# Kernel optimization log

Measured on AMD Instinct MI355X. Metric: run time of the kernel, lower is better.

The kernel has to match this reference:

```python
import jax, jax.numpy as jnp
import numpy as np

NUM_GRAPHS = 1024


def gcn_conv(x, src, dst, W, b, num_nodes):
    # PyG GCNConv: x' = D^{-1/2}(A+I)D^{-1/2} X W + b, self-loops added.
    h = x @ W  # [N, out]
    deg = jax.ops.segment_sum(jnp.ones_like(dst, dtype=h.dtype), dst, num_segments=num_nodes)
    dinv = jnp.where(deg > 0, jax.lax.rsqrt(deg), 0.0)
    norm = dinv[src] * dinv[dst]  # [E+N]
    msg = h[src] * norm[:, None]
    out = jax.ops.segment_sum(msg, dst, num_segments=num_nodes)
    return out + b


def setup_inputs() -> dict:
    key = jax.random.key(0)
    ks = jax.random.split(key, 16)
    N, E, F_IN, F_OUT = 100000, 1600000, 128, 256
    x = jax.random.normal(ks[0], (N, F_IN), dtype=jnp.float32)
    edge_index = jax.random.randint(ks[1], (2, E), 0, N, dtype=jnp.int64)
    batch = jnp.sort(jax.random.randint(ks[2], (N,), 0, NUM_GRAPHS, dtype=jnp.int64))

    def glorot(k, shape):
        lim = np.sqrt(6.0 / (shape[0] + shape[1]))
        return jax.random.uniform(k, shape, jnp.float32, -lim, lim)

    return {
        "x": x, "edge_index": edge_index, "batch": batch,
        "W1": glorot(ks[3], (F_IN, 16)), "b1": jnp.zeros((16,), jnp.float32),
        "W2": glorot(ks[4], (16, 32)), "b2": jnp.zeros((32,), jnp.float32),
        "W3": glorot(ks[5], (32, 64)), "b3": jnp.zeros((64,), jnp.float32),
        "L1_w": glorot(ks[6], (64, 256)), "L1_b": jnp.zeros((256,), jnp.float32),
        "L2_w": glorot(ks[7], (256, F_OUT)), "L2_b": jnp.zeros((F_OUT,), jnp.float32),
    }


def reference(x, edge_index, batch, W1, b1, W2, b2, W3, b3, L1_w, L1_b, L2_w, L2_b):
    N = x.shape[0]
    loops = jnp.arange(N, dtype=edge_index.dtype)
    src = jnp.concatenate([edge_index[0], loops])
    dst = jnp.concatenate([edge_index[1], loops])

    h = jax.nn.relu(gcn_conv(x, src, dst, W1, b1, N))
    h = jax.nn.relu(gcn_conv(h, src, dst, W2, b2, N))
    h = jax.nn.relu(gcn_conv(h, src, dst, W3, b3, N))

    pooled = jax.ops.segment_max(h, batch, num_segments=NUM_GRAPHS)  # [G, 64]
    pooled = jnp.where(jnp.isfinite(pooled), pooled, 0.0)  # empty segments -> 0

    z = jax.nn.relu(pooled @ L1_w + L1_b)
    return jax.nn.sigmoid(z @ L2_w + L2_b)
```

## Files before the change

### kernel.cpp

```cpp
#include <hip/hip_runtime.h>
#include <hip/hip_fp16.h>
#include <math.h>

#define NG 1024
#define EPB 2048
#define EPB_BIN 4096

static inline int cdiv_i(long long a, int b) { return (int)((a + b - 1) / b); }

union H8 { uint4 u; __half2 h[4]; };

__device__ inline void h8_to_f(uint4 uu, float* f) {
    H8 v; v.u = uu;
#pragma unroll
    for (int k = 0; k < 4; ++k) {
        float2 t = __half22float2(v.h[k]);
        f[2 * k] = t.x; f[2 * k + 1] = t.y;
    }
}
__device__ inline uint4 f_to_h8(const float* f) {
    H8 v;
#pragma unroll
    for (int k = 0; k < 4; ++k) v.h[k] = __floats2half2_rn(f[2 * k], f[2 * k + 1]);
    return v.u;
}

__global__ void zero_init(int* __restrict__ bcnt, unsigned* __restrict__ pooled) {
    int t = blockIdx.x * 256 + threadIdx.x;
    if (t < 256) bcnt[t] = 0;
    if (t < NG * 64) pooled[t] = 0;
}


__global__ void bucket_count(const int* __restrict__ dst, int* __restrict__ bcnt, int E) {
    __shared__ int h[256];
    int t = threadIdx.x;
    h[t] = 0;
    __syncthreads();
    int e0 = blockIdx.x * EPB;
#pragma unroll 4
    for (int k = 0; k < EPB / 256; ++k) {
        int e = e0 + k * 256 + t;
        if (e < E) atomicAdd(&h[dst[e] >> 9], 1);
    }
    __syncthreads();
    if (h[t] > 0) atomicAdd(&bcnt[t], h[t]);
}

__global__ void bucket_scan(const int* __restrict__ bcnt, int* __restrict__ bktbase,
                            int* __restrict__ bktcur, int* __restrict__ rowptr,
                            int NBKT, int N) {
    __shared__ int s[256];
    int t = threadIdx.x;
    int v = (t < NBKT) ? bcnt[t] : 0;
    s[t] = v;
    __syncthreads();
    for (int off = 1; off < 256; off <<= 1) {
        int u = (t >= off) ? s[t - off] : 0;
        __syncthreads();
        s[t] += u;
        __syncthreads();
    }
    int excl = s[t] - v;
    if (t < NBKT) { bktbase[t] = excl; bktcur[t] = excl; }
    if (t == 255) { bktbase[NBKT] = s[255]; rowptr[N] = s[255]; }
}

__global__ void bin_edges(const int* __restrict__ src, const int* __restrict__ dst,
                          int* __restrict__ bktcur, unsigned* __restrict__ binned, int E) {
    __shared__ int hist[256];
    __shared__ int sc[256];
    __shared__ int lofs[256];
    __shared__ int gbase[256];
    __shared__ int lcur[256];
    __shared__ unsigned stage[EPB_BIN];
    __shared__ int gaddr[EPB_BIN];
    int t = threadIdx.x;
    hist[t] = 0;
    __syncthreads();
    int e0 = blockIdx.x * EPB_BIN;
    int ne = E - e0; if (ne > EPB_BIN) ne = EPB_BIN;
    int myd[EPB_BIN / 256];
    int mys[EPB_BIN / 256];
#pragma unroll
    for (int k = 0; k < EPB_BIN / 256; ++k) {
        int e = e0 + k * 256 + t;
        if (e < E) {
            int d = dst[e];
            myd[k] = d;
            atomicAdd(&hist[d >> 9], 1);
        } else {
            myd[k] = -1;
        }
    }
#pragma unroll
    for (int k = 0; k < EPB_BIN / 256; ++k) {
        int e = e0 + k * 256 + t;
        mys[k] = (e < E) ? src[e] : 0;
    }
    __syncthreads();
    int v = hist[t];
    sc[t] = v;
    __syncthreads();
    for (int off = 1; off < 256; off <<= 1) {
        int u = (t >= off) ? sc[t - off] : 0;
        __syncthreads();
        sc[t] += u;
        __syncthreads();
    }
    lofs[t] = sc[t] - v;
    lcur[t] = sc[t] - v;
    if (v > 0) gbase[t] = atomicAdd(&bktcur[t], v);
    __syncthreads();
#pragma unroll
    for (int k = 0; k < EPB_BIN / 256; ++k) {
        int d = myd[k];
        if (d >= 0) {
            int b = d >> 9;
            int r = atomicAdd(&lcur[b], 1);
            stage[r] = ((unsigned)(d & 511) << 23) | (unsigned)mys[k];
            gaddr[r] = gbase[b] + (r - lofs[b]);
        }
    }
    __syncthreads();
    for (int j = t; j < ne; j += 256) binned[gaddr[j]] = stage[j];
}

__global__ void bucket_build(const int* __restrict__ bktbase, const unsigned* __restrict__ binned,
                             int* __restrict__ rowptr, float* __restrict__ dinv,
                             int* __restrict__ csr_src, int N) {
    __shared__ int degl[512];
    __shared__ int s[512];
    __shared__ int rp[512];
    __shared__ int cur[512];
    int t = threadIdx.x;
    int n0 = blockIdx.x << 9;
    degl[t] = 0;
    cur[t] = 0;
    __syncthreads();
    int base = bktbase[blockIdx.x], end = bktbase[blockIdx.x + 1];
    for (int j = base + t; j < end; j += 512) atomicAdd(&degl[binned[j] >> 23], 1);
    __syncthreads();
    int d = degl[t];
    s[t] = d;
    __syncthreads();
    for (int off = 1; off < 512; off <<= 1) {
        int u = (t >= off) ? s[t - off] : 0;
        __syncthreads();
        s[t] += u;
        __syncthreads();
    }
    rp[t] = base + s[t] - d;
    int i = n0 + t;
    if (i < N) {
        rowptr[i] = rp[t];
        dinv[i] = rsqrtf((float)(d + 1));
    }
    __syncthreads();
    for (int j = base + t; j < end; j += 512) {
        unsigned v = binned[j];
        int li = v >> 23;
        int slot = rp[li] + atomicAdd(&cur[li], 1);
        csr_src[slot] = (int)(v & 0x7FFFFFu);
    }
}

__global__ void gemm1(const float* __restrict__ x, const float* __restrict__ dinv,
                      const float* __restrict__ W, uint4* __restrict__ t1, int N) {
    __shared__ float Wl[128 * 16];
    int t = threadIdx.x;
    for (int k = t; k < 128 * 16; k += 256) Wl[k] = W[k];
    __syncthreads();
    int i = blockIdx.x * 256 + t;
    if (i >= N) return;
    const float4* x4 = (const float4*)(x + (size_t)i * 128);
    const float4* W4 = (const float4*)Wl;
    float4 a[4];
#pragma unroll
    for (int c = 0; c < 4; ++c) a[c] = make_float4(0.f, 0.f, 0.f, 0.f);
#pragma unroll 4
    for (int k4 = 0; k4 < 32; ++k4) {
        float4 v = x4[k4];
#pragma unroll
        for (int kk = 0; kk < 4; ++kk) {
            float xk = (kk == 0) ? v.x : (kk == 1) ? v.y : (kk == 2) ? v.z : v.w;
            const float4* Wr = W4 + (k4 * 4 + kk) * 4;
#pragma unroll
            for (int c = 0; c < 4; ++c) {
                float4 w = Wr[c];
                a[c].x += xk * w.x; a[c].y += xk * w.y;
                a[c].z += xk * w.z; a[c].w += xk * w.w;
            }
        }
    }
    float di = dinv[i];
    float f[16];
#pragma unroll
    for (int c = 0; c < 4; ++c) {
        f[4 * c + 0] = di * a[c].x; f[4 * c + 1] = di * a[c].y;
        f[4 * c + 2] = di * a[c].z; f[4 * c + 3] = di * a[c].w;
    }
    t1[(size_t)i * 2]     = f_to_h8(f);
    t1[(size_t)i * 2 + 1] = f_to_h8(f + 8);
}

__global__ void gather16_epi(const int* __restrict__ rowptr, const int* __restrict__ csr_src,
                             const uint4* __restrict__ hs, const float* __restrict__ dinv,
                             const float* __restrict__ b, uint4* __restrict__ out, int N) {
    int tid = blockIdx.x * 256 + threadIdx.x;
    int i = tid >> 1, c = tid & 1;
    if (i >= N) return;
    float acc[8];
    h8_to_f(hs[(size_t)i * 2 + c], acc);
    int j = rowptr[i], end = rowptr[i + 1];
    for (; j + 1 < end; j += 2) {
        int s0 = csr_src[j], s1 = csr_src[j + 1];
        uint4 u0 = hs[(size_t)s0 * 2 + c];
        uint4 u1 = hs[(size_t)s1 * 2 + c];
        float v0[8], v1[8];
        h8_to_f(u0, v0);
        h8_to_f(u1, v1);
#pragma unroll
        for (int k = 0; k < 8; ++k) acc[k] += v0[k] + v1[k];
    }
    if (j < end) {
        int s0 = csr_src[j];
        float v0[8];
        h8_to_f(hs[(size_t)s0 * 2 + c], v0);
#pragma unroll
        for (int k = 0; k < 8; ++k) acc[k] += v0[k];
    }
    float di = dinv[i];
#pragma unroll
    for (int k = 0; k < 8; ++k) acc[k] = di * fmaxf(di * acc[k] + b[c * 8 + k], 0.f);
    out[(size_t)i * 2 + c] = f_to_h8(acc);
}

__global__ void gather_gemm2(const int* __restrict__ rowptr, const int* __restrict__ csr_src,
                             const uint4* __restrict__ p1, const float* __restrict__ dinv,
                             const float* __restrict__ W, const float* __restrict__ b,
                             uint4* __restrict__ p2a, uint4* __restrict__ p2b, int N) {
    __shared__ float Wl[16 * 32];
    __shared__ float bl[32];
    int t = threadIdx.x;
    for (int k = t; k < 16 * 32; k += 256) Wl[k] = W[k];
    if (t < 32) bl[t] = b[t];
    __syncthreads();
    int i = blockIdx.x * 256 + t;
    if (i >= N) return;
    float f[16];
    h8_to_f(p1[(size_t)i * 2], f);
    h8_to_f(p1[(size_t)i * 2 + 1], f + 8);
    int j = rowptr[i], end = rowptr[i + 1];
    for (; j + 1 < end; j += 2) {
        int s0 = csr_src[j], s1 = csr_src[j + 1];
        uint4 a0 = p1[(size_t)s0 * 2], a1 = p1[(size_t)s0 * 2 + 1];
        uint4 b0 = p1[(size_t)s1 * 2], b1 = p1[(size_t)s1 * 2 + 1];
        float v[16], u[16];
        h8_to_f(a0, v); h8_to_f(a1, v + 8);
        h8_to_f(b0, u); h8_to_f(b1, u + 8);
#pragma unroll
        for (int k = 0; k < 16; ++k) f[k] += v[k] + u[k];
    }
    if (j < end) {
        int s0 = csr_src[j];
        float v[16];
        h8_to_f(p1[(size_t)s0 * 2], v);
        h8_to_f(p1[(size_t)s0 * 2 + 1], v + 8);
#pragma unroll
        for (int k = 0; k < 16; ++k) f[k] += v[k];
    }
    const float4* W4 = (const float4*)Wl;
    float4 a[8];
#pragma unroll
    for (int c = 0; c < 8; ++c) a[c] = make_float4(0.f, 0.f, 0.f, 0.f);
#pragma unroll
    for (int k = 0; k < 16; ++k) {
        float xk = f[k];
        const float4* Wr = W4 + k * 8;
#pragma unroll
        for (int c = 0; c < 8; ++c) {
            float4 w = Wr[c];
            a[c].x += xk * w.x; a[c].y += xk * w.y;
            a[c].z += xk * w.z; a[c].w += xk * w.w;
        }
    }
    float di = dinv[i];
    float o[32];
#pragma unroll
    for (int c = 0; c < 8; ++c) {
        o[4 * c + 0] = di * fmaxf(di * a[c].x + bl[4 * c + 0], 0.f);
        o[4 * c + 1] = di * fmaxf(di * a[c].y + bl[4 * c + 1], 0.f);
        o[4 * c + 2] = di * fmaxf(di * a[c].z + bl[4 * c + 2], 0.f);
        o[4 * c + 3] = di * fmaxf(di * a[c].w + bl[4 * c + 3], 0.f);
    }
    p2a[(size_t)i * 2]     = f_to_h8(o);
    p2a[(size_t)i * 2 + 1] = f_to_h8(o + 8);
    p2b[(size_t)i * 2]     = f_to_h8(o + 16);
    p2b[(size_t)i * 2 + 1] = f_to_h8(o + 24);
}

__global__ void gather_gemm3_pool(const int* __restrict__ rowptr, const int* __restrict__ csr_src,
                                  const uint4* __restrict__ p2a, const uint4* __restrict__ p2b,
                                  const float* __restrict__ dinv, const float* __restrict__ W,
                                  const float* __restrict__ b, const int* __restrict__ batch,
                                  unsigned* __restrict__ pooled, int N) {
    __shared__ float Wl[32 * 64];
    __shared__ float bl[64];
    __shared__ float fl[128][33];
    __shared__ float pl[128][65];
    __shared__ int bt[128];
    int t = threadIdx.x;
    for (int k = t; k < 32 * 64; k += 256) Wl[k] = W[k];
    if (t < 64) bl[t] = b[t];
    int i0 = blockIdx.x * 128;
    if (t < 128) {
        int i = i0 + t;
        bt[t] = (i < N) ? batch[i] : -1;
    }
    int il = t & 127, c = t >> 7;
    int i = i0 + il;
    if (i < N) {
        const uint4* P = c ? p2b : p2a;
        float acc[16];
        uint4 s0 = P[(size_t)i * 2], s1 = P[(size_t)i * 2 + 1];
        h8_to_f(s0, acc);
        h8_to_f(s1, acc + 8);
        int j = rowptr[i], end = rowptr[i + 1];
        for (; j + 1 < end; j += 2) {
            int n0 = csr_src[j], n1 = csr_src[j + 1];
            uint4 a0 = P[(size_t)n0 * 2], a1 = P[(size_t)n0 * 2 + 1];
            uint4 b0 = P[(size_t)n1 * 2], b1 = P[(size_t)n1 * 2 + 1];
            float v[16], u[16];
            h8_to_f(a0, v); h8_to_f(a1, v + 8);
            h8_to_f(b0, u); h8_to_f(b1, u + 8);
#pragma unroll
            for (int k = 0; k < 16; ++k) acc[k] += v[k] + u[k];
        }
        if (j < end) {
            int n0 = csr_src[j];
            float v[16];
            h8_to_f(P[(size_t)n0 * 2], v);
            h8_to_f(P[(size_t)n0 * 2 + 1], v + 8);
#pragma unroll
            for (int k = 0; k < 16; ++k) acc[k] += v[k];
        }
#pragma unroll
        for (int k = 0; k < 16; ++k) fl[il][c * 16 + k] = acc[k];
    }
    __syncthreads();
    if (i < N) {
        const float4* W4 = (const float4*)Wl;
        float4 a[8];
#pragma unroll
        for (int cc = 0; cc < 8; ++cc) a[cc] = make_float4(0.f, 0.f, 0.f, 0.f);
#pragma unroll 4
        for (int k = 0; k < 32; ++k) {
            float xk = fl[il][k];
            const float4* Wr = W4 + k * 16 + c * 8;
#pragma unroll
            for (int cc = 0; cc < 8; ++cc) {
                float4 w = Wr[cc];
                a[cc].x += xk * w.x; a[cc].y += xk * w.y;
                a[cc].z += xk * w.z; a[cc].w += xk * w.w;
            }
        }
        float di = dinv[i];
        int fb = c * 32;
#pragma unroll
        for (int cc = 0; cc < 8; ++cc) {
            pl[il][fb + 4 * cc + 0] = fmaxf(di * a[cc].x + bl[fb + 4 * cc + 0], 0.f);
            pl[il][fb + 4 * cc + 1] = fmaxf(di * a[cc].y + bl[fb + 4 * cc + 1], 0.f);
            pl[il][fb + 4 * cc + 2] = fmaxf(di * a[cc].z + bl[fb + 4 * cc + 2], 0.f);
            pl[il][fb + 4 * cc + 3] = fmaxf(di * a[cc].w + bl[fb + 4 * cc + 3], 0.f);
        }
    }
    __syncthreads();
    int f = t & 63, q = t >> 6;
    int prevb = -1;
    float run = 0.f;
    for (int k = 0; k < 32; ++k) {
        int il2 = q * 32 + k;
        int bg = bt[il2];
        if (bg < 0) break;
        float v = pl[il2][f];
        if (bg != prevb) {
            if (prevb >= 0) atomicMax(&pooled[prevb * 64 + f], __float_as_uint(run));
            prevb = bg;
            run = v;
        } else {
            run = fmaxf(run, v);
        }
    }
    if (prevb >= 0) atomicMax(&pooled[prevb * 64 + f], __float_as_uint(run));
}

__global__ void head4(const float* __restrict__ pooled, const float* __restrict__ w1,
                      const float* __restrict__ bb1, const float* __restrict__ w2,
                      const float* __restrict__ bb2, float* __restrict__ out) {
    __shared__ float p[4][64];
    __shared__ float z[4][256];
    int g0 = blockIdx.x * 4, t = threadIdx.x;
    p[t >> 6][t & 63] = pooled[(g0 + (t >> 6)) * 64 + (t & 63)];
    __syncthreads();
    float s[4];
#pragma unroll
    for (int q = 0; q < 4; ++q) s[q] = bb1[t];
    for (int k = 0; k < 64; ++k) {
        float w = w1[k * 256 + t];
#pragma unroll
        for (int q = 0; q < 4; ++q) s[q] += p[q][k] * w;
    }
#pragma unroll
    for (int q = 0; q < 4; ++q) z[q][t] = fmaxf(s[q], 0.f);
    __syncthreads();
    float s2[4];
#pragma unroll
    for (int q = 0; q < 4; ++q) s2[q] = bb2[t];
#pragma unroll 4
    for (int k = 0; k < 256; ++k) {
        float w = w2[k * 256 + t];
#pragma unroll
        for (int q = 0; q < 4; ++q) s2[q] += z[q][k] * w;
    }
#pragma unroll
    for (int q = 0; q < 4; ++q) out[(g0 + q) * 256 + t] = 1.f / (1.f + expf(-s2[q]));
}

extern "C" void kernel_launch(void* const* d_in, const int* in_sizes, int n_in,
                              void* d_out, int out_size, void* d_ws, size_t ws_size,
                              hipStream_t stream) {
    const float* x   = (const float*)d_in[0];
    const int* ei    = (const int*)d_in[1];
    const int* batch = (const int*)d_in[2];
    const float* W1  = (const float*)d_in[3];
    const float* b1  = (const float*)d_in[4];
    const float* W2  = (const float*)d_in[5];
    const float* b2  = (const float*)d_in[6];
    const float* W3  = (const float*)d_in[7];
    const float* b3  = (const float*)d_in[8];
    const float* L1w = (const float*)d_in[9];
    const float* L1b = (const float*)d_in[10];
    const float* L2w = (const float*)d_in[11];
    const float* L2b = (const float*)d_in[12];

    const int N = in_sizes[0] / 128;
    const int E = in_sizes[1] / 2;
    const int* srcp = ei;
    const int* dstp = ei + E;
    const int NB = cdiv_i(N, 256);
    const int NBKT = cdiv_i(N, 512);

    char* w = (char*)d_ws;
    auto carve = [&](size_t bytes) { char* p = w; w += (bytes + 15) & ~(size_t)15; return p; };
    int*   bcnt    = (int*)carve(256 * 4);
    int*   bktbase = (int*)carve(257 * 4);
    int*   bktcur  = (int*)carve(256 * 4);
    int*   rowptr  = (int*)carve((size_t)(N + 1) * 4);
    int*   csr_src = (int*)carve((size_t)E * 4);
    float* dinv    = (float*)carve((size_t)N * 4);
    uint4* t1      = (uint4*)carve((size_t)N * 32);
    uint4* p1      = (uint4*)carve((size_t)N * 32);
    uint4* p2a     = (uint4*)carve((size_t)N * 32);
    uint4* p2b     = (uint4*)carve((size_t)N * 32);
    unsigned* binned = (unsigned*)carve((size_t)E * 4);
    unsigned* pooled = (unsigned*)carve((size_t)NG * 64 * 4);

    zero_init<<<cdiv_i(NG * 64, 256), 256, 0, stream>>>(bcnt, pooled);

    bucket_count<<<cdiv_i(E, EPB), 256, 0, stream>>>(dstp, bcnt, E);
    bucket_scan<<<1, 256, 0, stream>>>(bcnt, bktbase, bktcur, rowptr, NBKT, N);
    bin_edges<<<cdiv_i(E, EPB_BIN), 256, 0, stream>>>(srcp, dstp, bktcur, binned, E);
    bucket_build<<<NBKT, 512, 0, stream>>>(bktbase, binned, rowptr, dinv, csr_src, N);

    const int GG = cdiv_i((long long)N * 2, 256);

    gemm1<<<NB, 256, 0, stream>>>(x, dinv, W1, t1, N);
    gather16_epi<<<GG, 256, 0, stream>>>(rowptr, csr_src, t1, dinv, b1, p1, N);

    gather_gemm2<<<NB, 256, 0, stream>>>(rowptr, csr_src, p1, dinv, W2, b2, p2a, p2b, N);

    gather_gemm3_pool<<<cdiv_i(N, 128), 256, 0, stream>>>(
        rowptr, csr_src, p2a, p2b, dinv, W3, b3, batch, pooled, N);

    head4<<<NG / 4, 256, 0, stream>>>((const float*)pooled, L1w, L1b, L2w, L2b, (float*)d_out);
}
```

Before: 204.4 us.

## Split layer-3 gather out of fused gemm3+pool into two 16-wide gather passes

The fused layer-3 kernel, which gathered 32 half features per node and then ran the GEMM and max-pool, is split into two passes of the generic 16-wide gather kernel, one per half-feature buffer, plus a separate gemm3_pool kernel. Each gather pass touches a 3.2 MB feature table, which may give better cache hit rates, and the gather gets the 2-threads-per-node layout with higher occupancy than the old kernel, which was heavy on shared memory. In exchange it adds two kernel launches, reads the CSR twice, and writes and rereads two intermediate buffers.

```diff
diff --git a/kernel.cpp b/kernel.cpp
--- a/kernel.cpp
+++ b/kernel.cpp
@@ -204,9 +204,10 @@
     t1[(size_t)i * 2 + 1] = f_to_h8(f + 8);
 }
 
-__global__ void gather16_epi(const int* __restrict__ rowptr, const int* __restrict__ csr_src,
-                             const uint4* __restrict__ hs, const float* __restrict__ dinv,
-                             const float* __restrict__ b, uint4* __restrict__ out, int N) {
+template <bool EPI>
+__global__ void gather16(const int* __restrict__ rowptr, const int* __restrict__ csr_src,
+                         const uint4* __restrict__ hs, const float* __restrict__ dinv,
+                         const float* __restrict__ b, uint4* __restrict__ out, int N) {
     int tid = blockIdx.x * 256 + threadIdx.x;
     int i = tid >> 1, c = tid & 1;
     if (i >= N) return;
@@ -230,9 +231,11 @@
 #pragma unroll
         for (int k = 0; k < 8; ++k) acc[k] += v0[k];
     }
-    float di = dinv[i];
-#pragma unroll
-    for (int k = 0; k < 8; ++k) acc[k] = di * fmaxf(di * acc[k] + b[c * 8 + k], 0.f);
+    if (EPI) {
+        float di = dinv[i];
+#pragma unroll
+        for (int k = 0; k < 8; ++k) acc[k] = di * fmaxf(di * acc[k] + b[c * 8 + k], 0.f);
+    }
     out[(size_t)i * 2 + c] = f_to_h8(acc);
 }
 
@@ -300,14 +303,12 @@
     p2b[(size_t)i * 2 + 1] = f_to_h8(o + 24);
 }
 
-__global__ void gather_gemm3_pool(const int* __restrict__ rowptr, const int* __restrict__ csr_src,
-                                  const uint4* __restrict__ p2a, const uint4* __restrict__ p2b,
-                                  const float* __restrict__ dinv, const float* __restrict__ W,
-                                  const float* __restrict__ b, const int* __restrict__ batch,
-                                  unsigned* __restrict__ pooled, int N) {
+__global__ void gemm3_pool(const uint4* __restrict__ g3a, const uint4* __restrict__ g3b,
+                           const float* __restrict__ dinv, const float* __restrict__ W,
+                           const float* __restrict__ b, const int* __restrict__ batch,
+                           unsigned* __restrict__ pooled, int N) {
     __shared__ float Wl[32 * 64];
     __shared__ float bl[64];
-    __shared__ float fl[128][33];
     __shared__ float pl[128][65];
     __shared__ int bt[128];
     int t = threadIdx.x;
@@ -318,45 +319,22 @@
         int i = i0 + t;
         bt[t] = (i < N) ? batch[i] : -1;
     }
+    __syncthreads();
     int il = t & 127, c = t >> 7;
     int i = i0 + il;
     if (i < N) {
-        const uint4* P = c ? p2b : p2a;
-        float acc[16];
-        uint4 s0 = P[(size_t)i * 2], s1 = P[(size_t)i * 2 + 1];
-        h8_to_f(s0, acc);
-        h8_to_f(s1, acc + 8);
-        int j = rowptr[i], end = rowptr[i + 1];
-        for (; j + 1 < end; j += 2) {
-            int n0 = csr_src[j], n1 = csr_src[j + 1];
-            uint4 a0 = P[(size_t)n0 * 2], a1 = P[(size_t)n0 * 2 + 1];
-            uint4 b0 = P[(size_t)n1 * 2], b1 = P[(size_t)n1 * 2 + 1];
-            float v[16], u[16];
-            h8_to_f(a0, v); h8_to_f(a1, v + 8);
-            h8_to_f(b0, u); h8_to_f(b1, u + 8);
-#pragma unroll
-            for (int k = 0; k < 16; ++k) acc[k] += v[k] + u[k];
-        }
-        if (j < end) {
-            int n0 = csr_src[j];
-            float v[16];
-            h8_to_f(P[(size_t)n0 * 2], v);
-            h8_to_f(P[(size_t)n0 * 2 + 1], v + 8);
-#pragma unroll
-            for (int k = 0; k < 16; ++k) acc[k] += v[k];
-        }
-#pragma unroll
-        for (int k = 0; k < 16; ++k) fl[il][c * 16 + k] = acc[k];
-    }
-    __syncthreads();
-    if (i < N) {
+        float f[32];
+        h8_to_f(g3a[(size_t)i * 2], f);
+        h8_to_f(g3a[(size_t)i * 2 + 1], f + 8);
+        h8_to_f(g3b[(size_t)i * 2], f + 16);
+        h8_to_f(g3b[(size_t)i * 2 + 1], f + 24);
         const float4* W4 = (const float4*)Wl;
         float4 a[8];
 #pragma unroll
         for (int cc = 0; cc < 8; ++cc) a[cc] = make_float4(0.f, 0.f, 0.f, 0.f);
 #pragma unroll 4
         for (int k = 0; k < 32; ++k) {
-            float xk = fl[il][k];
+            float xk = f[k];
             const float4* Wr = W4 + k * 16 + c * 8;
 #pragma unroll
             for (int cc = 0; cc < 8; ++cc) {
@@ -463,6 +441,8 @@
     uint4* p1      = (uint4*)carve((size_t)N * 32);
     uint4* p2a     = (uint4*)carve((size_t)N * 32);
     uint4* p2b     = (uint4*)carve((size_t)N * 32);
+    uint4* g3a     = (uint4*)carve((size_t)N * 32);
+    uint4* g3b     = (uint4*)carve((size_t)N * 32);
     unsigned* binned = (unsigned*)carve((size_t)E * 4);
     unsigned* pooled = (unsigned*)carve((size_t)NG * 64 * 4);
 
@@ -476,12 +456,13 @@
     const int GG = cdiv_i((long long)N * 2, 256);
 
     gemm1<<<NB, 256, 0, stream>>>(x, dinv, W1, t1, N);
-    gather16_epi<<<GG, 256, 0, stream>>>(rowptr, csr_src, t1, dinv, b1, p1, N);
+    gather16<true><<<GG, 256, 0, stream>>>(rowptr, csr_src, t1, dinv, b1, p1, N);
 
     gather_gemm2<<<NB, 256, 0, stream>>>(rowptr, csr_src, p1, dinv, W2, b2, p2a, p2b, N);
 
-    gather_gemm3_pool<<<cdiv_i(N, 128), 256, 0, stream>>>(
-        rowptr, csr_src, p2a, p2b, dinv, W3, b3, batch, pooled, N);
+    gather16<false><<<GG, 256, 0, stream>>>(rowptr, csr_src, p2a, nullptr, nullptr, g3a, N);
+    gather16<false><<<GG, 256, 0, stream>>>(rowptr, csr_src, p2b, nullptr, nullptr, g3b, N);
+    gemm3_pool<<<cdiv_i(N, 128), 256, 0, stream>>>(g3a, g3b, dinv, W3, b3, batch, pooled, N);
 
     head4<<<NG / 4, 256, 0, stream>>>((const float*)pooled, L1w, L1b, L2w, L2b, (float*)d_out);
 }
```

Result: no change. 203.5 us (-0.4%).
